# Performance work log

Measured on AMD Instinct MI355X. Metric: run time of the kernel, lower is better.

The kernel has to match this reference:

```python
import jax, jax.numpy as jnp
import numpy as np

N = 100000
E = 1600000
D = 128

def setup_inputs() -> dict:
    key = jax.random.key(0)
    ks = jax.random.split(key, 8)
    s = 1.0 / np.sqrt(D)
    x = jax.random.normal(ks[0], (N, D), dtype=jnp.float32)
    Wl1 = jax.random.uniform(ks[1], (D, D), jnp.float32, -s, s)
    bl1 = jnp.zeros((D,), jnp.float32)
    Wr1 = jax.random.uniform(ks[2], (D, D), jnp.float32, -s, s)
    Wl2 = jax.random.uniform(ks[3], (D, D), jnp.float32, -s, s)
    bl2 = jnp.zeros((D,), jnp.float32)
    Wr2 = jax.random.uniform(ks[4], (D, D), jnp.float32, -s, s)
    edge_index = jax.random.randint(ks[5], (2, E), 0, N, dtype=jnp.int64)
    return {"x": x, "Wl1": Wl1, "bl1": bl1, "Wr1": Wr1,
            "Wl2": Wl2, "bl2": bl2, "Wr2": Wr2, "edge_index": edge_index}

def _sage_layer(x, src, dst, Wl, bl, Wr, num_nodes):
    # mean aggregation of source features onto destination nodes
    msg = x[src]                                               # [E, D] gather
    ssum = jax.ops.segment_sum(msg, dst, num_segments=num_nodes)
    deg = jax.ops.segment_sum(jnp.ones((src.shape[0], 1), x.dtype), dst,
                              num_segments=num_nodes)
    agg = ssum / jnp.maximum(deg, 1.0)
    # out = lin_l(agg) + lin_r(x); lin_l has bias, lin_r has none (PyG SAGEConv)
    return agg @ Wl + bl + x @ Wr

def reference(x, Wl1, bl1, Wr1, Wl2, bl2, Wr2, edge_index):
    src, dst = edge_index[0], edge_index[1]
    n = x.shape[0]
    h = jax.nn.relu(_sage_layer(x, src, dst, Wl1, bl1, Wr1, n))
    # dropout is identity at inference
    h = jax.nn.relu(_sage_layer(h, src, dst, Wl2, bl2, Wr2, n))
    return h
```

## Files before the change

kernel.cpp:

```cpp
#include <hip/hip_runtime.h>
#include <cstdint>

typedef float f4 __attribute__((ext_vector_type(4)));
typedef float f2 __attribute__((ext_vector_type(2)));
typedef short bfv8 __attribute__((ext_vector_type(8)));

__device__ inline f4 f4_zero(){ f4 v = {0.f,0.f,0.f,0.f}; return v; }
__device__ inline f2 f2_zero(){ f2 v = {0.f,0.f}; return v; }

__device__ inline uint32_t f2bf(float f){
    uint32_t u = __float_as_uint(f);
    return (u + 0x7fffu + ((u >> 16) & 1u)) >> 16;
}
__device__ inline uint32_t pack_bf2(float a, float b){
    return f2bf(a) | (f2bf(b) << 16);
}
__device__ inline f2 bf2_unpack(uint32_t v){
    f2 r;
    r[0] = __uint_as_float(v << 16);
    r[1] = __uint_as_float(v & 0xffff0000u);
    return r;
}

#define PB 256

__device__ inline bool detect_is64(const uint32_t* p, int* sflag){
    int t = threadIdx.x;
    if (t == 0) *sflag = 0;
    __syncthreads();
    int local = 0;
    for (int i = t; i < 2048; i += blockDim.x)
        if (p[2*i + 1] != 0u) local = 1;
    if (local) atomicOr(sflag, 1);
    __syncthreads();
    return *sflag == 0;
}

__global__ __launch_bounds__(256) void k_tobf16(const f4* __restrict__ in,
                                                uint2* __restrict__ out, int n4){
    int i = blockIdx.x * 256 + threadIdx.x;
    if (i >= n4) return;
    f4 v = in[i];
    uint2 o;
    o.x = pack_bf2(v[0], v[1]);
    o.y = pack_bf2(v[2], v[3]);
    out[i] = o;
}

__global__ __launch_bounds__(1024) void k_hist(const void* __restrict__ eidx, int E, int NB,
                                               int* __restrict__ blkhist){
    __shared__ int lh[1024];
    __shared__ int dflag;
    bool is64 = detect_is64((const uint32_t*)eidx, &dflag);
    int t = threadIdx.x, blk = blockIdx.x;
    for (int i = t; i < NB; i += 1024) lh[i] = 0;
    __syncthreads();
    int R = (E + PB - 1) / PB;
    int s = blk * R, e_end = s + R < E ? s + R : E;
    const uint32_t* p32 = (const uint32_t*)eidx;
    const int*      pi  = (const int*)eidx;
    for (int e = s + t; e < e_end; e += 1024){
        int d = is64 ? (int)p32[2*(size_t)(E + e)] : pi[(size_t)E + e];
        atomicAdd(&lh[d >> 7], 1);
    }
    __syncthreads();
    for (int i = t; i < NB; i += 1024)
        blkhist[(size_t)i * PB + blk] = lh[i];
}

__global__ __launch_bounds__(1024) void k_offsets(const int* __restrict__ blkhist,
                                                  int NB,
                                                  int* __restrict__ coff,
                                                  int* __restrict__ offs){
    __shared__ int tot_s[1024];
    __shared__ int excl_s[1024];
    __shared__ int ws[16];
    int t = threadIdx.x, lane = t & 63, w = t >> 6;
    int v = 0;
    if (t < NB){
        const int4* row = (const int4*)(blkhist + (size_t)t * PB);
        #pragma unroll 8
        for (int i = 0; i < PB/4; ++i){
            int4 q = row[i];
            v += q.x + q.y + q.z + q.w;
        }
    }
    tot_s[t] = v;
    __syncthreads();
    int x = tot_s[t];
    int vv = x;
    #pragma unroll
    for (int off = 1; off < 64; off <<= 1){
        int u = __shfl_up(x, off, 64);
        if (lane >= off) x += u;
    }
    if (lane == 63) ws[w] = x;
    __syncthreads();
    if (w == 0 && lane < 16){
        int y = ws[lane];
        #pragma unroll
        for (int off = 1; off < 16; off <<= 1){
            int u = __shfl_up(y, off, 64);
            if (lane >= off) y += u;
        }
        ws[lane] = y;
    }
    __syncthreads();
    int incl = x + (w ? ws[w - 1] : 0);
    int excl = incl - vv;
    excl_s[t] = excl;
    if (t < NB)      coff[t] = excl;
    if (t == NB - 1) coff[NB] = incl;
    __syncthreads();
    if (t < NB){
        const int4* row  = (const int4*)(blkhist + (size_t)t * PB);
        int4*       orow = (int4*)(offs + (size_t)t * PB);
        int run = excl_s[t];
        #pragma unroll 8
        for (int i = 0; i < PB/4; ++i){
            int4 q = row[i];
            int4 o;
            o.x = run; run += q.x;
            o.y = run; run += q.y;
            o.z = run; run += q.z;
            o.w = run; run += q.w;
            orow[i] = o;
        }
    }
}

__global__ __launch_bounds__(1024) void k_scatter(const void* __restrict__ eidx, int E, int NB,
                                                  const int* __restrict__ offs,
                                                  uint32_t* __restrict__ bucketed){
    __shared__ int cur[1024];
    __shared__ int dflag;
    bool is64 = detect_is64((const uint32_t*)eidx, &dflag);
    int t = threadIdx.x, blk = blockIdx.x;
    for (int i = t; i < NB; i += 1024) cur[i] = offs[(size_t)i * PB + blk];
    __syncthreads();
    int R = (E + PB - 1) / PB;
    int s = blk * R, e_end = s + R < E ? s + R : E;
    const uint32_t* p32 = (const uint32_t*)eidx;
    const int*      pi  = (const int*)eidx;
    for (int e = s + t; e < e_end; e += 1024){
        int sv, dv;
        if (is64){ sv = (int)p32[2*(size_t)e]; dv = (int)p32[2*(size_t)(E + e)]; }
        else     { sv = pi[e];                 dv = pi[(size_t)E + e]; }
        int b = dv >> 7;
        int pos = atomicAdd(&cur[b], 1);
        bucketed[pos] = ((uint32_t)(dv & 127) << 17) | (uint32_t)sv;
    }
}

__global__ __launch_bounds__(1024) void k_bucketsort(const uint32_t* __restrict__ bucketed,
                                                     const int* __restrict__ coff,
                                                     int* __restrict__ esrc,
                                                     int* __restrict__ rowptr,
                                                     int N, int E, int NB){
    __shared__ int hist[128], cur[128], wtot[2];
    int b = blockIdx.x, t = threadIdx.x;
    if (t < 128) hist[t] = 0;
    __syncthreads();
    int s = coff[b], e_end = coff[b + 1];
    for (int i = s + t; i < e_end; i += 1024)
        atomicAdd(&hist[bucketed[i] >> 17], 1);
    __syncthreads();
    int x = 0, v = 0;
    if (t < 128){
        int lane = t & 63;
        v = hist[t]; x = v;
        #pragma unroll
        for (int off = 1; off < 64; off <<= 1){
            int u = __shfl_up(x, off, 64);
            if (lane >= off) x += u;
        }
        if (lane == 63) wtot[t >> 6] = x;
    }
    __syncthreads();
    if (t < 128){
        int w = t >> 6;
        int excl = x - v + (w ? wtot[0] : 0);
        int abs0 = s + excl;
        cur[t] = abs0;
        int node = b * 128 + t;
        if (node < N) rowptr[node] = abs0;
    }
    if (b == NB - 1 && t == 0) rowptr[N] = E;
    __syncthreads();
    for (int i = s + t; i < e_end; i += 1024){
        uint32_t val = bucketed[i];
        int r = (int)(val >> 17);
        int pos = atomicAdd(&cur[r], 1);
        esrc[pos] = (int)(val & 0x1FFFFu);
    }
}

__global__ __launch_bounds__(256) void k_aggregate(const uint32_t* __restrict__ featb,
                                                   const int* __restrict__ rowptr,
                                                   const int* __restrict__ esrc,
                                                   uint32_t* __restrict__ aggb, int N){
    int node = blockIdx.x * 4 + (threadIdx.x >> 6);
    if (node >= N) return;
    int lane = threadIdx.x & 63;
    int half = lane >> 5;
    int l8   = lane & 31;
    int b = rowptr[node], e = rowptr[node + 1];
    f2 lo0=f2_zero(),lo1=f2_zero(),lo2=f2_zero(),lo3=f2_zero();
    f2 lo4=f2_zero(),lo5=f2_zero(),lo6=f2_zero(),lo7=f2_zero();
    f2 hi0=f2_zero(),hi1=f2_zero(),hi2=f2_zero(),hi3=f2_zero();
    f2 hi4=f2_zero(),hi5=f2_zero(),hi6=f2_zero(),hi7=f2_zero();
    for (int base = b; base < e; base += 64){
        int m = e - base; if (m > 64) m = 64;
        int idx = (lane < m) ? esrc[base + lane] : 0;
        int j = 0;
        for (; j + 16 <= m; j += 16){
            int s0 = __shfl(idx, j      + half, 64);
            int s1 = __shfl(idx, j + 2  + half, 64);
            int s2 = __shfl(idx, j + 4  + half, 64);
            int s3 = __shfl(idx, j + 6  + half, 64);
            int s4 = __shfl(idx, j + 8  + half, 64);
            int s5 = __shfl(idx, j + 10 + half, 64);
            int s6 = __shfl(idx, j + 12 + half, 64);
            int s7 = __shfl(idx, j + 14 + half, 64);
            uint2 g0 = *(const uint2*)(featb + (size_t)s0 * 64 + l8 * 2);
            uint2 g1 = *(const uint2*)(featb + (size_t)s1 * 64 + l8 * 2);
            uint2 g2 = *(const uint2*)(featb + (size_t)s2 * 64 + l8 * 2);
            uint2 g3 = *(const uint2*)(featb + (size_t)s3 * 64 + l8 * 2);
            uint2 g4 = *(const uint2*)(featb + (size_t)s4 * 64 + l8 * 2);
            uint2 g5 = *(const uint2*)(featb + (size_t)s5 * 64 + l8 * 2);
            uint2 g6 = *(const uint2*)(featb + (size_t)s6 * 64 + l8 * 2);
            uint2 g7 = *(const uint2*)(featb + (size_t)s7 * 64 + l8 * 2);
            lo0 += bf2_unpack(g0.x); hi0 += bf2_unpack(g0.y);
            lo1 += bf2_unpack(g1.x); hi1 += bf2_unpack(g1.y);
            lo2 += bf2_unpack(g2.x); hi2 += bf2_unpack(g2.y);
            lo3 += bf2_unpack(g3.x); hi3 += bf2_unpack(g3.y);
            lo4 += bf2_unpack(g4.x); hi4 += bf2_unpack(g4.y);
            lo5 += bf2_unpack(g5.x); hi5 += bf2_unpack(g5.y);
            lo6 += bf2_unpack(g6.x); hi6 += bf2_unpack(g6.y);
            lo7 += bf2_unpack(g7.x); hi7 += bf2_unpack(g7.y);
        }
        if (j + 8 <= m){
            int s0 = __shfl(idx, j     + half, 64);
            int s1 = __shfl(idx, j + 2 + half, 64);
            int s2 = __shfl(idx, j + 4 + half, 64);
            int s3 = __shfl(idx, j + 6 + half, 64);
            uint2 g0 = *(const uint2*)(featb + (size_t)s0 * 64 + l8 * 2);
            uint2 g1 = *(const uint2*)(featb + (size_t)s1 * 64 + l8 * 2);
            uint2 g2 = *(const uint2*)(featb + (size_t)s2 * 64 + l8 * 2);
            uint2 g3 = *(const uint2*)(featb + (size_t)s3 * 64 + l8 * 2);
            lo0 += bf2_unpack(g0.x); hi0 += bf2_unpack(g0.y);
            lo1 += bf2_unpack(g1.x); hi1 += bf2_unpack(g1.y);
            lo2 += bf2_unpack(g2.x); hi2 += bf2_unpack(g2.y);
            lo3 += bf2_unpack(g3.x); hi3 += bf2_unpack(g3.y);
            j += 8;
        }
        for (; j < m; j += 2){
            int jj = j + half;
            int s0 = __shfl(idx, jj < m ? jj : j, 64);
            uint2 g = *(const uint2*)(featb + (size_t)s0 * 64 + l8 * 2);
            if (jj < m){ lo0 += bf2_unpack(g.x); hi0 += bf2_unpack(g.y); }
        }
    }
    f2 lo = ((lo0 + lo1) + (lo2 + lo3)) + ((lo4 + lo5) + (lo6 + lo7));
    f2 hi = ((hi0 + hi1) + (hi2 + hi3)) + ((hi4 + hi5) + (hi6 + hi7));
    lo[0] += __shfl_xor(lo[0], 32, 64);
    lo[1] += __shfl_xor(lo[1], 32, 64);
    hi[0] += __shfl_xor(hi[0], 32, 64);
    hi[1] += __shfl_xor(hi[1], 32, 64);
    if (half == 0){
        int deg = e - b;
        float scl = 1.0f / (float)(deg > 1 ? deg : 1);
        uint2 o;
        o.x = pack_bf2(lo[0] * scl, lo[1] * scl);
        o.y = pack_bf2(hi[0] * scl, hi[1] * scl);
        *(uint2*)(aggb + (size_t)node * 64 + l8 * 2) = o;
    }
}

__global__ __launch_bounds__(256) void k_wprep(const float* __restrict__ Wl,
                                               const float* __restrict__ Wr,
                                               uint32_t* __restrict__ Bsw){
    int t = blockIdx.x * 256 + threadIdx.x;
    int s = t >> 9, ct = (t >> 6) & 7, l = t & 63;
    int k0 = s * 32 + (l >> 4) * 8;
    int c  = ct * 16 + (l & 15);
    unsigned short e[8];
    #pragma unroll
    for (int j = 0; j < 8; ++j){
        int k = k0 + j;
        float v = (k < 128) ? Wl[(size_t)k * 128 + c] : Wr[(size_t)(k - 128) * 128 + c];
        e[j] = (unsigned short)f2bf(v);
    }
    uint32_t* o = Bsw + (size_t)t * 4;
    o[0] = (uint32_t)e[0] | ((uint32_t)e[1] << 16);
    o[1] = (uint32_t)e[2] | ((uint32_t)e[3] << 16);
    o[2] = (uint32_t)e[4] | ((uint32_t)e[5] << 16);
    o[3] = (uint32_t)e[6] | ((uint32_t)e[7] << 16);
}

__global__ __launch_bounds__(256) void k_sage_mfma(
    const uint32_t* __restrict__ A1b, const uint32_t* __restrict__ A2b,
    const uint32_t* __restrict__ Bsw, const float* __restrict__ bias,
    float* __restrict__ outf, uint32_t* __restrict__ outbf, int M)
{
    int tid = threadIdx.x;
    int w = tid >> 6, l = tid & 63;
    int l15 = l & 15, l4 = l >> 4;
    int row = blockIdx.x * 64 + w * 16 + l15;
    int rowc = row < M ? row : M - 1;
    const char* a1p = (const char*)(A1b + (size_t)rowc * 64) + l4 * 16;
    const char* a2p = (const char*)(A2b + (size_t)rowc * 64) + l4 * 16;
    const char* bp  = (const char*)Bsw + (size_t)l * 16;

    f4 acc[8];
    #pragma unroll
    for (int ct = 0; ct < 8; ++ct) acc[ct] = f4_zero();

    #pragma unroll
    for (int s = 0; s < 8; ++s){
        bfv8 a = *(const bfv8*)((s < 4 ? a1p : a2p) + (s & 3) * 64);
        #pragma unroll
        for (int ct = 0; ct < 8; ++ct){
            bfv8 b = *(const bfv8*)(bp + (size_t)(s * 8 + ct) * 1024);
            acc[ct] = __builtin_amdgcn_mfma_f32_16x16x32_bf16(a, b, acc[ct], 0, 0, 0);
        }
    }

    int orow0 = blockIdx.x * 64 + w * 16 + l4 * 4;
    #pragma unroll
    for (int ct = 0; ct < 8; ++ct){
        int col = ct * 16 + l15;
        float bb = bias[col];
        #pragma unroll
        for (int r = 0; r < 4; ++r){
            int orow = orow0 + r;
            if (orow < M){
                float v = acc[ct][r] + bb;
                v = v > 0.f ? v : 0.f;
                if (outf)  outf[(size_t)orow * 128 + col] = v;
                if (outbf) ((unsigned short*)outbf)[(size_t)orow * 128 + col] =
                               (unsigned short)f2bf(v);
            }
        }
    }
}

extern "C" void kernel_launch(void* const* d_in, const int* in_sizes, int n_in,
                              void* d_out, int out_size, void* d_ws, size_t ws_size,
                              hipStream_t stream) {
    const float* x    = (const float*)d_in[0];
    const float* Wl1  = (const float*)d_in[1];
    const float* bl1  = (const float*)d_in[2];
    const float* Wr1  = (const float*)d_in[3];
    const float* Wl2  = (const float*)d_in[4];
    const float* bl2  = (const float*)d_in[5];
    const float* Wr2  = (const float*)d_in[6];
    const void*  eidx = d_in[7];
    float* out = (float*)d_out;

    const int N  = in_sizes[0] / 128;
    const int E  = in_sizes[7] / 2;
    const int NB = (N + 127) >> 7;

    char* ws = (char*)d_ws;
    size_t off = 0;
    auto alloc = [&](size_t bytes) -> void* {
        void* p = ws + off;
        off += (bytes + 255) & ~(size_t)255;
        return p;
    };
    int*      blkhist  = (int*)     alloc((size_t)NB * PB * 4);
    int*      coff     = (int*)     alloc((size_t)(NB + 1) * 4);
    int*      offs     = (int*)     alloc((size_t)NB * PB * 4);
    int*      esrc     = (int*)     alloc((size_t)E * 4);
    int*      rowptr   = (int*)     alloc((size_t)(N + 1) * 4);
    uint32_t* bsw1     = (uint32_t*)alloc(65536);
    uint32_t* bsw2     = (uint32_t*)alloc(65536);
    size_t uA = (size_t)E * 4 > (size_t)N * 256 ? (size_t)E * 4 : (size_t)N * 256;
    uint32_t* unionA   = (uint32_t*)alloc(uA);
    uint32_t* bucketed = unionA;
    uint32_t* aggb     = unionA;
    uint32_t* unionB   = (uint32_t*)alloc((size_t)N * 256);
    uint32_t* xbf      = unionB;
    uint32_t* hbf      = unionB;

    const int GB = (N + 63) / 64;

    k_tobf16    <<<(N * 32 + 255) / 256, 256, 0, stream>>>((const f4*)x, (uint2*)xbf, N * 32);
    k_wprep     <<<16, 256, 0, stream>>>(Wl1, Wr1, bsw1);
    k_wprep     <<<16, 256, 0, stream>>>(Wl2, Wr2, bsw2);
    k_hist      <<<PB, 1024, 0, stream>>>(eidx, E, NB, blkhist);
    k_offsets   <<<1, 1024, 0, stream>>>(blkhist, NB, coff, offs);
    k_scatter   <<<PB, 1024, 0, stream>>>(eidx, E, NB, offs, bucketed);
    k_bucketsort<<<NB, 1024, 0, stream>>>(bucketed, coff, esrc, rowptr, N, E, NB);

    k_aggregate<<<(N + 3) / 4, 256, 0, stream>>>(xbf, rowptr, esrc, aggb, N);
    k_sage_mfma<<<GB, 256, 0, stream>>>(aggb, xbf, bsw1, bl1, nullptr, hbf, N);

    k_aggregate<<<(N + 3) / 4, 256, 0, stream>>>(hbf, rowptr, esrc, aggb, N);
    k_sage_mfma<<<GB, 256, 0, stream>>>(aggb, hbf, bsw2, bl2, out, nullptr, N);
}
```

Baseline: 422.8 us.

## Split single-block offset scan into parallel three-kernel reduce-scan-propagate

The single-block k_offsets kernel, in which each of up to 1024 threads serially walked a 256-entry row of the block histogram, is replaced by three kernels. k_btot reduces each bucket row in parallel (one block per bucket), k_bscan scans the bucket totals in one block, and k_boff computes per-block offsets with a wave-level scan across NB blocks. This removes a serial, single-CU bottleneck, at the cost of two extra kernel launches and an extra pass over blkhist.

After: 353.2 us. 1.2x faster.

```diff
diff --git a/kernel.cpp b/kernel.cpp
--- a/kernel.cpp
+++ b/kernel.cpp
@@ -68,32 +68,29 @@
         blkhist[(size_t)i * PB + blk] = lh[i];
 }
 
-__global__ __launch_bounds__(1024) void k_offsets(const int* __restrict__ blkhist,
-                                                  int NB,
-                                                  int* __restrict__ coff,
-                                                  int* __restrict__ offs){
-    __shared__ int tot_s[1024];
-    __shared__ int excl_s[1024];
-    __shared__ int ws[16];
+__global__ __launch_bounds__(PB) void k_btot(const int* __restrict__ blkhist,
+                                             int* __restrict__ tot){
+    int b = blockIdx.x, t = threadIdx.x, lane = t & 63, w = t >> 6;
+    int v = blkhist[(size_t)b * PB + t];
+    #pragma unroll
+    for (int off = 32; off; off >>= 1) v += __shfl_down(v, off, 64);
+    __shared__ int ws[4];
+    if (lane == 0) ws[w] = v;
+    __syncthreads();
+    if (t == 0) tot[b] = ws[0] + ws[1] + ws[2] + ws[3];
+}
+
+__global__ __launch_bounds__(1024) void k_bscan(const int* __restrict__ tot, int n,
+                                                int* __restrict__ coff){
     int t = threadIdx.x, lane = t & 63, w = t >> 6;
-    int v = 0;
-    if (t < NB){
-        const int4* row = (const int4*)(blkhist + (size_t)t * PB);
-        #pragma unroll 8
-        for (int i = 0; i < PB/4; ++i){
-            int4 q = row[i];
-            v += q.x + q.y + q.z + q.w;
-        }
-    }
-    tot_s[t] = v;
-    __syncthreads();
-    int x = tot_s[t];
-    int vv = x;
+    int v = (t < n) ? tot[t] : 0;
+    int x = v;
     #pragma unroll
     for (int off = 1; off < 64; off <<= 1){
         int u = __shfl_up(x, off, 64);
         if (lane >= off) x += u;
     }
+    __shared__ int ws[16];
     if (lane == 63) ws[w] = x;
     __syncthreads();
     if (w == 0 && lane < 16){
@@ -107,26 +104,27 @@
     }
     __syncthreads();
     int incl = x + (w ? ws[w - 1] : 0);
-    int excl = incl - vv;
-    excl_s[t] = excl;
-    if (t < NB)      coff[t] = excl;
-    if (t == NB - 1) coff[NB] = incl;
-    __syncthreads();
-    if (t < NB){
-        const int4* row  = (const int4*)(blkhist + (size_t)t * PB);
-        int4*       orow = (int4*)(offs + (size_t)t * PB);
-        int run = excl_s[t];
-        #pragma unroll 8
-        for (int i = 0; i < PB/4; ++i){
-            int4 q = row[i];
-            int4 o;
-            o.x = run; run += q.x;
-            o.y = run; run += q.y;
-            o.z = run; run += q.z;
-            o.w = run; run += q.w;
-            orow[i] = o;
-        }
-    }
+    if (t < n)     coff[t] = incl - v;
+    if (t == n - 1) coff[n] = incl;
+}
+
+__global__ __launch_bounds__(PB) void k_boff(const int* __restrict__ blkhist,
+                                             const int* __restrict__ coff,
+                                             int* __restrict__ offs){
+    int b = blockIdx.x, t = threadIdx.x, lane = t & 63, w = t >> 6;
+    int h = blkhist[(size_t)b * PB + t];
+    int x = h;
+    #pragma unroll
+    for (int off = 1; off < 64; off <<= 1){
+        int u = __shfl_up(x, off, 64);
+        if (lane >= off) x += u;
+    }
+    __shared__ int ws[4];
+    if (lane == 63) ws[w] = x;
+    __syncthreads();
+    int add = 0;
+    for (int j = 0; j < w; ++j) add += ws[j];
+    offs[(size_t)b * PB + t] = coff[b] + add + x - h;
 }
 
 __global__ __launch_bounds__(1024) void k_scatter(const void* __restrict__ eidx, int E, int NB,
@@ -370,6 +368,7 @@
         return p;
     };
     int*      blkhist  = (int*)     alloc((size_t)NB * PB * 4);
+    int*      tot      = (int*)     alloc((size_t)NB * 4);
     int*      coff     = (int*)     alloc((size_t)(NB + 1) * 4);
     int*      offs     = (int*)     alloc((size_t)NB * PB * 4);
     int*      esrc     = (int*)     alloc((size_t)E * 4);
@@ -390,7 +389,9 @@
     k_wprep     <<<16, 256, 0, stream>>>(Wl1, Wr1, bsw1);
     k_wprep     <<<16, 256, 0, stream>>>(Wl2, Wr2, bsw2);
     k_hist      <<<PB, 1024, 0, stream>>>(eidx, E, NB, blkhist);
-    k_offsets   <<<1, 1024, 0, stream>>>(blkhist, NB, coff, offs);
+    k_btot      <<<NB, PB,   0, stream>>>(blkhist, tot);
+    k_bscan     <<<1, 1024,  0, stream>>>(tot, NB, coff);
+    k_boff      <<<NB, PB,   0, stream>>>(blkhist, coff, offs);
     k_scatter   <<<PB, 1024, 0, stream>>>(eidx, E, NB, offs, bucketed);
     k_bucketsort<<<NB, 1024, 0, stream>>>(bucketed, coff, esrc, rowptr, N, E, NB);
 
```
